# Kernel tuning notes

Measured on AMD Instinct MI355X. Metric: run time of the kernel, lower is better.

## Reference

```python
import jax, jax.numpy as jnp
import numpy as np

N = 100000; E = 1600000; D_IN = 9; HID = 16; HEADS = 8; D = HID * HEADS; G = 1000
NEG_SLOPE = 0.2; LN_EPS = 1e-5


def _gat_conv(x, src, dst, W, a_src, a_dst, b, heads, ch):
    # PyG GATConv (eval mode, self-loops already appended to src/dst)
    h = (x @ W).reshape(-1, heads, ch)                   # [N,H,C]
    al_s = (h * a_src).sum(-1)                           # [N,H]
    al_d = (h * a_dst).sum(-1)                           # [N,H]
    e = al_s[src] + al_d[dst]                            # [Et,H]
    e = jnp.where(e > 0, e, NEG_SLOPE * e)               # LeakyReLU(0.2)
    m = jax.ops.segment_max(e, dst, num_segments=N)      # per-dst softmax
    alpha = jnp.exp(e - m[dst])
    denom = jax.ops.segment_sum(alpha, dst, num_segments=N)
    alpha = alpha / (denom[dst] + 1e-16)
    out = jax.ops.segment_sum(h[src] * alpha[:, :, None], dst, num_segments=N)
    return out.reshape(-1, heads * ch) + b


def _ln_graph(x, g, b):
    # PyG LayerNorm, mode='graph', batch=None: normalize over all nodes+channels
    mu = x.mean()
    var = jnp.mean((x - mu) ** 2)
    return (x - mu) / jnp.sqrt(var + LN_EPS) * g + b


def setup_inputs() -> dict:
    key = jax.random.key(0)
    ks = jax.random.split(key, 20)
    s = 0.1
    p = lambda i, shape: jax.random.normal(ks[i], shape, jnp.float32) * s
    return {
        "x": jax.random.normal(ks[0], (N, D_IN), jnp.float32),
        "edge_index": jax.random.randint(ks[1], (2, E), 0, N),
        "batch": jnp.sort(jax.random.randint(ks[2], (N,), 0, G)),
        "W1": p(3, (D_IN, D)), "a_src1": p(4, (HEADS, HID)), "a_dst1": p(5, (HEADS, HID)), "b1": jnp.zeros((D,), jnp.float32),
        "W2": p(6, (D, D)), "a_src2": p(7, (1, D)), "a_dst2": p(8, (1, D)), "b2": jnp.zeros((D,), jnp.float32),
        "fc1_w": p(9, (D, D)), "fc1_b": jnp.zeros((D,), jnp.float32),
        "fc2_w": p(10, (D, D)), "fc2_b": jnp.zeros((D,), jnp.float32),
        "fc3_w": p(11, (D, D)), "fc3_b": jnp.zeros((D,), jnp.float32),
        "fc4_w": p(12, (D, D)), "fc4_b": jnp.zeros((D,), jnp.float32),
        "g1": jnp.ones((D,), jnp.float32), "beta1": jnp.zeros((D,), jnp.float32),
        "g2": jnp.ones((D,), jnp.float32), "beta2": jnp.zeros((D,), jnp.float32),
        "fcf_w": p(13, (D, 1)), "fcf_b": jnp.zeros((1,), jnp.float32),
    }


def reference(x, edge_index, batch, W1, a_src1, a_dst1, b1, W2, a_src2, a_dst2, b2,
              fc1_w, fc1_b, fc2_w, fc2_b, fc3_w, fc3_b, fc4_w, fc4_b,
              g1, beta1, g2, beta2, fcf_w, fcf_b):
    loops = jnp.arange(N)
    src = jnp.concatenate([edge_index[0], loops])
    dst = jnp.concatenate([edge_index[1], loops])
    h = jax.nn.relu(_gat_conv(x, src, dst, W1, a_src1, a_dst1, b1, HEADS, HID))
    hc = h
    h = jax.nn.relu(h @ fc1_w + fc1_b)
    h = jax.nn.relu(h @ fc2_w + fc2_b + hc)
    h = _ln_graph(h, g1, beta1)
    hc = h
    h = _gat_conv(h, src, dst, W2, a_src2, a_dst2, b2, 1, D)
    h = jax.nn.relu(h @ fc3_w + fc3_b)
    h = h @ fc4_w + fc4_b + hc
    h = _ln_graph(h, g2, beta2)
    h = h @ fcf_w + fcf_b                                # [N,1]
    sums = jax.ops.segment_sum(h, batch, num_segments=G)
    cnt = jax.ops.segment_sum(jnp.ones((N,), h.dtype), batch, num_segments=G)
    return sums / jnp.maximum(cnt, 1.0)[:, None]          # global_mean_pool -> [G,1]
```

## Files before the change

kernel.cpp:

```cpp
#include <hip/hip_runtime.h>
#include <cstdint>

#define NN 100000
#define NE 1600000
#define DI 9
#define DD 128
#define NH 8
#define NG 1000
#define LOG2E 1.44269504f

#define NBK 3125
#define NBLK 256
#define EPB (NE/NBLK)

typedef unsigned int uint;
typedef __attribute__((ext_vector_type(8))) short bf16x8;
typedef __attribute__((ext_vector_type(4))) float f32x4;

__device__ __forceinline__ float leaky(float x){ return fmaxf(x, 0.2f*x); }
__device__ __forceinline__ uint f2bf(float f){
  uint u = __float_as_uint(f);
  return (u + 0x7fffu + ((u>>16)&1u)) >> 16;
}
__device__ __forceinline__ float bflo(uint p){ return __uint_as_float(p << 16); }
__device__ __forceinline__ float bfhi(uint p){ return __uint_as_float(p & 0xffff0000u); }
__device__ __forceinline__ uint packbf(float a, float b){ return f2bf(a) | (f2bf(b)<<16); }
__device__ __forceinline__ float rdlanef(float v, int l){
  return __uint_as_float((uint)__builtin_amdgcn_readlane((int)__float_as_uint(v), l));
}

union U16 { uint4 u; bf16x8 v; };
__device__ __forceinline__ bf16x8 ld8(const uint* p){ U16 t; t.u = *(const uint4*)p; return t.v; }

__global__ __launch_bounds__(512) void k_hist(const int* __restrict__ dst, int* __restrict__ hist){
  __shared__ int h[NBK];
  for (int i = threadIdx.x; i < NBK; i += 512) h[i] = 0;
  __syncthreads();
  int blk = blockIdx.x;
  int beg = blk*EPB, end = beg + EPB;
  for (int i = beg + threadIdx.x; i < end; i += 512)
    atomicAdd(&h[dst[i] >> 5], 1);
  __syncthreads();
  for (int b = threadIdx.x; b < NBK; b += 512) hist[(size_t)blk*NBK + b] = h[b];
}

__global__ __launch_bounds__(256) void k_bsum(int* __restrict__ hist, int* __restrict__ bsum){
  int b = blockIdx.x*256 + threadIdx.x;
  if (b >= NBK) return;
  int run = 0;
  for (int k = 0; k < NBLK; ++k){
    int t = hist[(size_t)k*NBK + b];
    hist[(size_t)k*NBK + b] = run;
    run += t;
  }
  bsum[b] = run;
}

__global__ __launch_bounds__(1024) void k_bscan(const int* __restrict__ bsum, int* __restrict__ bbase){
  __shared__ int sh[1024];
  __shared__ int carry;
  if (threadIdx.x == 0) carry = 0;
  __syncthreads();
  for (int c0 = 0; c0 < NBK; c0 += 1024){
    int i = c0 + threadIdx.x;
    int v = (i < NBK) ? bsum[i] : 0;
    sh[threadIdx.x] = v;
    __syncthreads();
    for (int off = 1; off < 1024; off <<= 1){
      int t = (threadIdx.x >= off) ? sh[threadIdx.x-off] : 0;
      __syncthreads();
      sh[threadIdx.x] += t;
      __syncthreads();
    }
    if (i < NBK) bbase[i] = carry + sh[threadIdx.x] - v;
    __syncthreads();
    if (threadIdx.x == 0) carry += sh[1023];
    __syncthreads();
  }
}

__global__ __launch_bounds__(512) void k_part(const int* __restrict__ src, const int* __restrict__ dst,
    const int* __restrict__ hist, const int* __restrict__ bbase, uint* __restrict__ ebuf){
  __shared__ int cur[NBK];
  int blk = blockIdx.x;
  for (int b = threadIdx.x; b < NBK; b += 512)
    cur[b] = hist[(size_t)blk*NBK + b] + bbase[b];
  __syncthreads();
  int beg = blk*EPB, end = beg + EPB;
  for (int i = beg + threadIdx.x; i < end; i += 512){
    int d = dst[i], s = src[i];
    int b = d >> 5;
    int p = atomicAdd(&cur[b], 1);
    ebuf[p] = (uint)s | ((uint)(d & 31) << 26);
  }
}

__global__ __launch_bounds__(64) void k_fin(const uint* __restrict__ ebuf, const int* __restrict__ bbase,
    const int* __restrict__ bsum, int* __restrict__ rowptr, int* __restrict__ col){
  __shared__ int cnt32[32];
  __shared__ int exc[32];
  int b = blockIdx.x;
  int lane = threadIdx.x;
  if (lane < 32) cnt32[lane] = 0;
  __syncthreads();
  int base = bbase[b], n = bsum[b];
  for (int i = lane; i < n; i += 64)
    atomicAdd(&cnt32[ebuf[base+i] >> 26], 1);
  __syncthreads();
  if (lane == 0){
    int run = 0;
    for (int d = 0; d < 32; ++d){
      int t = cnt32[d];
      exc[d] = run;
      rowptr[b*32 + d] = base + run;
      run += t;
    }
  }
  __syncthreads();
  if (lane < 32) cnt32[lane] = exc[lane];
  __syncthreads();
  for (int i = lane; i < n; i += 64){
    uint e = ebuf[base+i];
    int d = e >> 26;
    int r = atomicAdd(&cnt32[d], 1);
    col[base + r] = (int)(e & 0x03ffffffu);
  }
  if (b == 0 && lane == 0) rowptr[NN] = NE;
}

__global__ __launch_bounds__(64) void k_wconv5(const float* __restrict__ w0, const float* __restrict__ w1,
    const float* __restrict__ w2, const float* __restrict__ w3, const float* __restrict__ w4,
    uint* __restrict__ o0, uint* __restrict__ o1, uint* __restrict__ o2,
    uint* __restrict__ o3, uint* __restrict__ o4){
  int which = blockIdx.x >> 7;
  int n = blockIdx.x & 127;
  int t = threadIdx.x;
  const float* W = (which==0)?w0:(which==1)?w1:(which==2)?w2:(which==3)?w3:w4;
  uint* WT = (which==0)?o0:(which==1)?o1:(which==2)?o2:(which==3)?o3:o4;
  float a = W[(2*t)*DD + n];
  float b = W[(2*t+1)*DD + n];
  WT[n*64 + t] = packbf(a, b);
}

__global__ __launch_bounds__(128) void k_lin1(const float* __restrict__ x, const float* __restrict__ W1,
    const float* __restrict__ as1, const float* __restrict__ ad1,
    uint* __restrict__ t1b, float* __restrict__ al_s, float* __restrict__ al_d){
  int n = blockIdx.x;
  int c = threadIdx.x;
  const float* xr = x + n*DI;
  float t = 0.f;
  #pragma unroll
  for (int k = 0; k < DI; ++k) t = fmaf(xr[k], W1[k*DD+c], t);
  uint mybf = f2bf(t);
  uint pbf  = (uint)__shfl_xor((int)mybf, 1, 64);
  if (!(c & 1)) t1b[(size_t)n*64 + (c>>1)] = mybf | (pbf<<16);
  float vs = t * as1[c];
  float vd = t * ad1[c];
  #pragma unroll
  for (int m = 8; m >= 1; m >>= 1){ vs += __shfl_xor(vs, m, 16); vd += __shfl_xor(vd, m, 16); }
  if ((c & 15) == 0){
    al_s[n*NH + (c>>4)] = vs*LOG2E;
    al_d[n*NH + (c>>4)] = vd*LOG2E;
  }
}

__global__ __launch_bounds__(256) void k_gat1(const uint* __restrict__ t1b,
    const float* __restrict__ al_s, const float* __restrict__ al_d,
    const int* __restrict__ rowptr, const int* __restrict__ col,
    const float* __restrict__ b1, uint* __restrict__ outb){
  int n = blockIdx.x*4 + (threadIdx.x >> 6);
  if (n >= NN) return;
  uint lane = threadIdx.x & 63;
  uint h = lane >> 3;
  float ald = al_d[(uint)n*NH + h];
  float a0  = exp2f(leaky(al_s[(uint)n*NH + h] + ald));
  uint  ps  = t1b[(uint)n*64u + lane];
  float den = a0;
  float s0 = a0*bflo(ps), s1 = a0*bfhi(ps);
  int beg = rowptr[n], end = rowptr[n+1];
  for (int e = beg; e < end; e += 16){
    uint cs[16]; float ls[16]; uint pp[16];
    #pragma unroll
    for (int j = 0; j < 16; ++j) cs[j] = (uint)col[e + j];
    #pragma unroll
    for (int j = 0; j < 16; ++j){
      ls[j] = al_s[cs[j]*8u + h];
      pp[j] = t1b[cs[j]*64u + lane];
    }
    #pragma unroll
    for (int j = 0; j < 16; ++j){
      float a = (e + j < end) ? exp2f(leaky(ls[j] + ald)) : 0.f;
      den += a;
      s0 = fmaf(a, bflo(pp[j]), s0);
      s1 = fmaf(a, bfhi(pp[j]), s1);
    }
  }
  float inv = 1.f/(den + 1e-16f);
  float2 bb = ((const float2*)b1)[lane];
  outb[(uint)n*64u + lane] = packbf(fmaxf(s0*inv + bb.x, 0.f), fmaxf(s1*inv + bb.y, 0.f));
}

__global__ __launch_bounds__(256) void k_gat2(const uint* __restrict__ t2b,
    const float* __restrict__ al_s, const float* __restrict__ al_d,
    const int* __restrict__ rowptr, const int* __restrict__ col,
    const float* __restrict__ b2, uint* __restrict__ outb){
  int n = blockIdx.x*4 + (threadIdx.x >> 6);
  if (n >= NN) return;
  uint lane = threadIdx.x & 63;
  float ald = al_d[n];
  float a0  = exp2f(leaky(al_s[n] + ald));
  uint  ps  = t2b[(uint)n*64u + lane];
  float s0 = a0*bflo(ps), s1 = a0*bfhi(ps);
  float vden = 0.f;
  int beg = rowptr[n], end = rowptr[n+1];
  for (int e = beg; e < end; e += 64){
    int ej = e + (int)lane;
    uint  mc = (uint)col[ej];
    float ml = al_s[mc];
    float ma = (ej < end) ? exp2f(leaky(ml + ald)) : 0.f;
    vden += ma;
    int rem = end - e;
    #pragma unroll
    for (int jb = 0; jb < 4; ++jb){
      if (jb*16 < rem){
        #pragma unroll
        for (int j = 0; j < 16; ++j){
          int lsrc = jb*16 + j;
          float a = rdlanef(ma, lsrc);
          uint  c = (uint)__builtin_amdgcn_readlane((int)mc, lsrc);
          uint  p = t2b[c*64u + lane];
          s0 = fmaf(a, bflo(p), s0);
          s1 = fmaf(a, bfhi(p), s1);
        }
      }
    }
  }
  #pragma unroll
  for (int m = 32; m >= 1; m >>= 1) vden += __shfl_xor(vden, m, 64);
  float inv = 1.f/(a0 + vden + 1e-16f);
  float2 bb = ((const float2*)b2)[lane];
  outb[(uint)n*64u + lane] = packbf(s0*inv + bb.x, s1*inv + bb.y);
}

template<bool RELU, bool BIAS, bool RES, bool LNRED, bool AL2>
__global__ __launch_bounds__(256) void k_mfma(const uint* __restrict__ Xb, const uint* __restrict__ WTb,
    const float* __restrict__ bias, const uint* __restrict__ resb, uint* __restrict__ outb,
    float* __restrict__ pbuf, const float* __restrict__ avs, const float* __restrict__ avd,
    float* __restrict__ o_als, float* __restrict__ o_ald, int nrows){
  int lane = threadIdx.x & 63;
  int wid  = threadIdx.x >> 6;
  int m0 = blockIdx.x*128 + wid*32;
  int lr = lane & 15, hi4 = lane >> 4;
  f32x4 acc[2][8];
  #pragma unroll
  for (int a = 0; a < 2; ++a)
    #pragma unroll
    for (int c = 0; c < 8; ++c) acc[a][c] = (f32x4){0.f,0.f,0.f,0.f};
  int ra0 = m0 + lr;      if (ra0 > NN-1) ra0 = NN-1;
  int ra1 = m0 + 16 + lr; if (ra1 > NN-1) ra1 = NN-1;
  #pragma unroll
  for (int kk = 0; kk < 4; ++kk){
    int ko = kk*16 + hi4*4;
    bf16x8 a0 = ld8(Xb + (size_t)ra0*64 + ko);
    bf16x8 a1 = ld8(Xb + (size_t)ra1*64 + ko);
    #pragma unroll
    for (int c = 0; c < 8; ++c){
      bf16x8 b = ld8(WTb + (size_t)(c*16 + lr)*64 + ko);
      acc[0][c] = __builtin_amdgcn_mfma_f32_16x16x32_bf16(a0, b, acc[0][c], 0, 0, 0);
      acc[1][c] = __builtin_amdgcn_mfma_f32_16x16x32_bf16(a1, b, acc[1][c], 0, 0, 0);
    }
  }
  if (AL2){
    #pragma unroll
    for (int rg = 0; rg < 2; ++rg){
      #pragma unroll
      for (int r = 0; r < 4; ++r){
        float vs = 0.f, vd = 0.f;
        #pragma unroll
        for (int c = 0; c < 8; ++c){
          float v = acc[rg][c][r];
          vs = fmaf(v, avs[c*16 + lr], vs);
          vd = fmaf(v, avd[c*16 + lr], vd);
        }
        #pragma unroll
        for (int m = 8; m >= 1; m >>= 1){ vs += __shfl_xor(vs, m, 64); vd += __shfl_xor(vd, m, 64); }
        int row = m0 + rg*16 + hi4*4 + r;
        if (lr == 0 && row < nrows){ o_als[row] = vs*LOG2E; o_ald[row] = vd*LOG2E; }
      }
    }
  }
  bool evn = !(lane & 1);
  int cph = lr >> 1;
  float lns = 0.f, lnss = 0.f;
  #pragma unroll
  for (int rg = 0; rg < 2; ++rg){
    #pragma unroll
    for (int c = 0; c < 8; ++c){
      int cp = c*8 + cph;
      #pragma unroll
      for (int r = 0; r < 4; ++r){
        float v0 = acc[rg][c][r];
        float v1 = __shfl_xor(v0, 1, 64);
        int row = m0 + rg*16 + hi4*4 + r;
        if (evn && row < nrows){
          if (BIAS){ float2 bb = ((const float2*)bias)[cp]; v0 += bb.x; v1 += bb.y; }
          if (RES){ uint rr = resb[(size_t)row*64 + cp]; v0 += bflo(rr); v1 += bfhi(rr); }
          if (RELU){ v0 = fmaxf(v0, 0.f); v1 = fmaxf(v1, 0.f); }
          outb[(size_t)row*64 + cp] = packbf(v0, v1);
          if (LNRED){ lns += v0 + v1; lnss += v0*v0 + v1*v1; }
        }
      }
    }
  }
  if (LNRED){
    #pragma unroll
    for (int m = 32; m >= 1; m >>= 1){ lns += __shfl_xor(lns, m, 64); lnss += __shfl_xor(lnss, m, 64); }
    __shared__ float shred[8];
    if (lane == 0){ shred[wid*2] = lns; shred[wid*2+1] = lnss; }
    __syncthreads();
    if (threadIdx.x == 0){
      float S = 0.f, SS = 0.f;
      for (int w = 0; w < 4; ++w){ S += shred[2*w]; SS += shred[2*w+1]; }
      pbuf[blockIdx.x*2] = S; pbuf[blockIdx.x*2+1] = SS;
    }
  }
}

__global__ __launch_bounds__(256) void k_ln_stats(const float* __restrict__ pbuf, float* __restrict__ stats, int nb){
  float s = 0.f, ss = 0.f;
  for (int i = threadIdx.x; i < nb; i += 256){ s += pbuf[2*i]; ss += pbuf[2*i+1]; }
  #pragma unroll
  for (int m = 32; m >= 1; m >>= 1){ s += __shfl_xor(s, m, 64); ss += __shfl_xor(ss, m, 64); }
  __shared__ float sh[8];
  int wid = threadIdx.x >> 6, lane = threadIdx.x & 63;
  if (lane == 0){ sh[wid*2] = s; sh[wid*2+1] = ss; }
  __syncthreads();
  if (threadIdx.x == 0){
    float S = 0.f, SS = 0.f;
    for (int w = 0; w < 4; ++w){ S += sh[2*w]; SS += sh[2*w+1]; }
    const float inv = 1.f/((float)NN*(float)DD);
    float mu = S*inv;
    float var = SS*inv - mu*mu;
    stats[0] = mu;
    stats[1] = rsqrtf(var + 1e-5f);
  }
}

__global__ __launch_bounds__(256) void k_ln_apply_bf(uint* __restrict__ xb, const float* __restrict__ g,
    const float* __restrict__ be, const float* __restrict__ stats){
  const int n4 = NN*16;
  float mu = stats[0], rs = stats[1];
  uint4* x4 = (uint4*)xb;
  const float2* g2 = (const float2*)g;
  const float2* b2 = (const float2*)be;
  for (int i = blockIdx.x*256 + threadIdx.x; i < n4; i += gridDim.x*256){
    int cb = (i & 15)*4;
    uint4 u = x4[i];
    float2 ga = g2[cb],   gb = g2[cb+1], gc = g2[cb+2], gd = g2[cb+3];
    float2 ba = b2[cb],   bb = b2[cb+1], bc = b2[cb+2], bd = b2[cb+3];
    u.x = packbf((bflo(u.x)-mu)*rs*ga.x + ba.x, (bfhi(u.x)-mu)*rs*ga.y + ba.y);
    u.y = packbf((bflo(u.y)-mu)*rs*gb.x + bb.x, (bfhi(u.y)-mu)*rs*gb.y + bb.y);
    u.z = packbf((bflo(u.z)-mu)*rs*gc.x + bc.x, (bfhi(u.z)-mu)*rs*gc.y + bc.y);
    u.w = packbf((bflo(u.w)-mu)*rs*gd.x + bd.x, (bfhi(u.w)-mu)*rs*gd.y + bd.y);
    x4[i] = u;
  }
}

__global__ __launch_bounds__(256) void k_fdot_ln(const uint* __restrict__ xb, const float* __restrict__ g,
    const float* __restrict__ be, const float* __restrict__ stats,
    const float* __restrict__ fw, const float* __restrict__ fb, float* __restrict__ val){
  int n = blockIdx.x*4 + (threadIdx.x >> 6);
  if (n >= NN) return;
  int lane = threadIdx.x & 63;
  float mu = stats[0], rs = stats[1];
  uint p = xb[(size_t)n*64 + lane];
  float2 gg = ((const float2*)g)[lane];
  float2 bb = ((const float2*)be)[lane];
  float2 ww = ((const float2*)fw)[lane];
  float v = ((bflo(p)-mu)*rs*gg.x + bb.x)*ww.x + ((bfhi(p)-mu)*rs*gg.y + bb.y)*ww.y;
  #pragma unroll
  for (int m = 32; m >= 1; m >>= 1) v += __shfl_xor(v, m, 64);
  if (lane == 0) val[n] = v + fb[0];
}

__global__ __launch_bounds__(64) void k_pool(const float* __restrict__ val, const int* __restrict__ batch,
                                             float* __restrict__ out){
  int g = blockIdx.x;
  int lane = threadIdx.x;
  int lo = 0, hi = NN;
  while (lo < hi){ int mid = (lo+hi)>>1; if (batch[mid] < g) lo = mid+1; else hi = mid; }
  int start = lo;
  hi = NN;
  while (lo < hi){ int mid = (lo+hi)>>1; if (batch[mid] < g+1) lo = mid+1; else hi = mid; }
  int end = lo;
  float s = 0.f;
  for (int i = start + lane; i < end; i += 64) s += val[i];
  #pragma unroll
  for (int m = 32; m >= 1; m >>= 1) s += __shfl_xor(s, m, 64);
  if (lane == 0) out[g] = s / fmaxf((float)(end - start), 1.f);
}

extern "C" void kernel_launch(void* const* d_in, const int* in_sizes, int n_in,
                              void* d_out, int out_size, void* d_ws, size_t ws_size,
                              hipStream_t stream){
  const float* x   = (const float*)d_in[0];
  const int*   ei  = (const int*)d_in[1];
  const int* batch = (const int*)d_in[2];
  const float* W1  = (const float*)d_in[3];
  const float* as1 = (const float*)d_in[4];
  const float* ad1 = (const float*)d_in[5];
  const float* b1  = (const float*)d_in[6];
  const float* W2  = (const float*)d_in[7];
  const float* as2 = (const float*)d_in[8];
  const float* ad2 = (const float*)d_in[9];
  const float* b2  = (const float*)d_in[10];
  const float* fc1w= (const float*)d_in[11];
  const float* fc1b= (const float*)d_in[12];
  const float* fc2w= (const float*)d_in[13];
  const float* fc2b= (const float*)d_in[14];
  const float* fc3w= (const float*)d_in[15];
  const float* fc3b= (const float*)d_in[16];
  const float* fc4w= (const float*)d_in[17];
  const float* fc4b= (const float*)d_in[18];
  const float* g1  = (const float*)d_in[19];
  const float* be1 = (const float*)d_in[20];
  const float* g2  = (const float*)d_in[21];
  const float* be2 = (const float*)d_in[22];
  const float* fcw = (const float*)d_in[23];
  const float* fcb = (const float*)d_in[24];
  float* out = (float*)d_out;
  (void)in_sizes; (void)n_in; (void)out_size; (void)ws_size;

  char* ws = (char*)d_ws;
  size_t off = 0;
  auto alloc = [&](size_t bytes)->void*{
    void* p = ws + off;
    off += (bytes + 255) & ~(size_t)255;
    return p;
  };
  float* A    = (float*)alloc((size_t)NN*DD*4);
  float* B    = (float*)alloc((size_t)NN*DD*4);
  float* C    = (float*)alloc((size_t)NN*DD*4);
  float* als1 = (float*)alloc((size_t)NN*NH*4);
  float* ald1 = (float*)alloc((size_t)NN*NH*4);
  float* als2 = (float*)alloc((size_t)NN*4);
  float* ald2 = (float*)alloc((size_t)NN*4);
  float* escr = (float*)alloc((size_t)NE*4);
  int*   rowptr = (int*)alloc((size_t)(NN+1)*4);
  int*   col    = (int*)alloc((size_t)(NE+64)*4);
  int*   bsum   = (int*)alloc((size_t)NBK*4);
  int*   bbase  = (int*)alloc((size_t)NBK*4);
  float* pbuf   = (float*)alloc(1024*2*4);
  float* stats  = (float*)alloc(2*4);
  float* val    = (float*)alloc((size_t)NN*4);
  uint* wt_fc1  = (uint*)alloc((size_t)DD*64*4);
  uint* wt_fc2  = (uint*)alloc((size_t)DD*64*4);
  uint* wt_w2   = (uint*)alloc((size_t)DD*64*4);
  uint* wt_fc3  = (uint*)alloc((size_t)DD*64*4);
  uint* wt_fc4  = (uint*)alloc((size_t)DD*64*4);

  uint*  Ab     = (uint*)A;
  uint*  Bb     = (uint*)B;
  uint*  Cb     = (uint*)C;
  int*   hist   = (int*)A;
  uint*  ebuf   = (uint*)escr;

  const int* esrc = ei;
  const int* edst = ei + NE;

  hipMemsetAsync(col + NE, 0, 64*4, stream);

  k_hist <<<NBLK, 512, 0, stream>>>(edst, hist);
  k_bsum <<<(NBK+255)/256, 256, 0, stream>>>(hist, bsum);
  k_bscan<<<1, 1024, 0, stream>>>(bsum, bbase);
  k_part <<<NBLK, 512, 0, stream>>>(esrc, edst, hist, bbase, ebuf);
  k_fin  <<<NBK, 64, 0, stream>>>(ebuf, bbase, bsum, rowptr, col);

  k_wconv5<<<5*DD, 64, 0, stream>>>(fc1w, fc2w, W2, fc3w, fc4w,
                                    wt_fc1, wt_fc2, wt_w2, wt_fc3, wt_fc4);

  const int WB = (NN + 3)/4;
  const int GB = (NN + 127)/128;

  k_lin1<<<NN, 128, 0, stream>>>(x, W1, as1, ad1, Ab, als1, ald1);
  k_gat1<<<WB, 256, 0, stream>>>(Ab, als1, ald1, rowptr, col, b1, Bb);

  k_mfma<true,  true, false, false, false><<<GB, 256, 0, stream>>>(Bb, wt_fc1, fc1b, nullptr, Ab, nullptr, nullptr, nullptr, nullptr, nullptr, NN);
  k_mfma<true,  true, true,  true,  false><<<GB, 256, 0, stream>>>(Ab, wt_fc2, fc2b, Bb,      Cb, pbuf,    nullptr, nullptr, nullptr, nullptr, NN);

  k_ln_stats<<<1, 256, 0, stream>>>(pbuf, stats, GB);
  k_ln_apply_bf<<<1024, 256, 0, stream>>>(Cb, g1, be1, stats);

  k_mfma<false, false, false, false, true ><<<GB, 256, 0, stream>>>(Cb, wt_w2, nullptr, nullptr, Ab, nullptr, as2, ad2, als2, ald2, NN);
  k_gat2<<<WB, 256, 0, stream>>>(Ab, als2, ald2, rowptr, col, b2, Bb);

  k_mfma<true,  true, false, false, false><<<GB, 256, 0, stream>>>(Bb, wt_fc3, fc3b, nullptr, Ab, nullptr, nullptr, nullptr, nullptr, nullptr, NN);
  k_mfma<false, true, true,  true,  false><<<GB, 256, 0, stream>>>(Ab, wt_fc4, fc4b, Cb,      Bb, pbuf,    nullptr, nullptr, nullptr, nullptr, NN);

  k_ln_stats<<<1, 256, 0, stream>>>(pbuf, stats, GB);
  k_fdot_ln<<<WB, 256, 0, stream>>>(Bb, g2, be2, stats, fcw, fcb, val);
  k_pool<<<NG, 64, 0, stream>>>(val, batch, out);
}
```

Before: 477.8 us.

## Coarsen CSR radix buckets to 512 nodes and scan bucket offsets in shared memory

The CSR build now partitions edges into 196 buckets of 512 destination nodes instead of 3125 buckets of 32. That shrinks the per-block histograms, the bucket-sum pass and the bucket-offset scan (now a single 1024-wide pass). k_fin now runs 256 threads per bucket and computes the 512 per-node offsets with a parallel shared-memory prefix scan. The packed edge format moves to 20 bits of source and 9 bits of local destination. The gat2 column load is also clamped so tail lanes no longer read past the row end. The trade-off is fewer, larger blocks in k_fin, which may lower parallelism for that pass, and more atomic contention on each shared counter.

```diff
diff --git a/kernel.cpp b/kernel.cpp
--- a/kernel.cpp
+++ b/kernel.cpp
@@ -9,7 +9,7 @@
 #define NG 1000
 #define LOG2E 1.44269504f
 
-#define NBK 3125
+#define NBK 196
 #define NBLK 256
 #define EPB (NE/NBLK)
 
@@ -39,9 +39,9 @@
   int blk = blockIdx.x;
   int beg = blk*EPB, end = beg + EPB;
   for (int i = beg + threadIdx.x; i < end; i += 512)
-    atomicAdd(&h[dst[i] >> 5], 1);
-  __syncthreads();
-  for (int b = threadIdx.x; b < NBK; b += 512) hist[(size_t)blk*NBK + b] = h[b];
+    atomicAdd(&h[dst[i] >> 9], 1);
+  __syncthreads();
+  for (int b = threadIdx.x; b < NBK; b += 512) hist[blk*NBK + b] = h[b];
 }
 
 __global__ __launch_bounds__(256) void k_bsum(int* __restrict__ hist, int* __restrict__ bsum){
@@ -49,8 +49,8 @@
   if (b >= NBK) return;
   int run = 0;
   for (int k = 0; k < NBLK; ++k){
-    int t = hist[(size_t)k*NBK + b];
-    hist[(size_t)k*NBK + b] = run;
+    int t = hist[k*NBK + b];
+    hist[k*NBK + b] = run;
     run += t;
   }
   bsum[b] = run;
@@ -58,25 +58,17 @@
 
 __global__ __launch_bounds__(1024) void k_bscan(const int* __restrict__ bsum, int* __restrict__ bbase){
   __shared__ int sh[1024];
-  __shared__ int carry;
-  if (threadIdx.x == 0) carry = 0;
-  __syncthreads();
-  for (int c0 = 0; c0 < NBK; c0 += 1024){
-    int i = c0 + threadIdx.x;
-    int v = (i < NBK) ? bsum[i] : 0;
-    sh[threadIdx.x] = v;
+  int i = threadIdx.x;
+  int v = (i < NBK) ? bsum[i] : 0;
+  sh[i] = v;
+  __syncthreads();
+  for (int off = 1; off < 1024; off <<= 1){
+    int t = (i >= off) ? sh[i-off] : 0;
     __syncthreads();
-    for (int off = 1; off < 1024; off <<= 1){
-      int t = (threadIdx.x >= off) ? sh[threadIdx.x-off] : 0;
-      __syncthreads();
-      sh[threadIdx.x] += t;
-      __syncthreads();
-    }
-    if (i < NBK) bbase[i] = carry + sh[threadIdx.x] - v;
+    sh[i] += t;
     __syncthreads();
-    if (threadIdx.x == 0) carry += sh[1023];
-    __syncthreads();
-  }
+  }
+  if (i < NBK) bbase[i] = sh[i] - v;
 }
 
 __global__ __launch_bounds__(512) void k_part(const int* __restrict__ src, const int* __restrict__ dst,
@@ -84,48 +76,55 @@
   __shared__ int cur[NBK];
   int blk = blockIdx.x;
   for (int b = threadIdx.x; b < NBK; b += 512)
-    cur[b] = hist[(size_t)blk*NBK + b] + bbase[b];
+    cur[b] = hist[blk*NBK + b] + bbase[b];
   __syncthreads();
   int beg = blk*EPB, end = beg + EPB;
   for (int i = beg + threadIdx.x; i < end; i += 512){
     int d = dst[i], s = src[i];
-    int b = d >> 5;
+    int b = d >> 9;
     int p = atomicAdd(&cur[b], 1);
-    ebuf[p] = (uint)s | ((uint)(d & 31) << 26);
-  }
-}
-
-__global__ __launch_bounds__(64) void k_fin(const uint* __restrict__ ebuf, const int* __restrict__ bbase,
+    ebuf[p] = (uint)s | ((uint)(d & 511) << 20);
+  }
+}
+
+__global__ __launch_bounds__(256) void k_fin(const uint* __restrict__ ebuf, const int* __restrict__ bbase,
     const int* __restrict__ bsum, int* __restrict__ rowptr, int* __restrict__ col){
-  __shared__ int cnt32[32];
-  __shared__ int exc[32];
+  __shared__ int cnt[512];
+  __shared__ int sc[256];
   int b = blockIdx.x;
-  int lane = threadIdx.x;
-  if (lane < 32) cnt32[lane] = 0;
+  int t = threadIdx.x;
+  int nb0 = b*512;
+  int nodes = NN - nb0; if (nodes > 512) nodes = 512;
+  cnt[t] = 0; cnt[t+256] = 0;
   __syncthreads();
   int base = bbase[b], n = bsum[b];
-  for (int i = lane; i < n; i += 64)
-    atomicAdd(&cnt32[ebuf[base+i] >> 26], 1);
-  __syncthreads();
-  if (lane == 0){
-    int run = 0;
-    for (int d = 0; d < 32; ++d){
-      int t = cnt32[d];
-      exc[d] = run;
-      rowptr[b*32 + d] = base + run;
-      run += t;
-    }
-  }
-  __syncthreads();
-  if (lane < 32) cnt32[lane] = exc[lane];
-  __syncthreads();
-  for (int i = lane; i < n; i += 64){
+  for (int i = t; i < n; i += 256)
+    atomicAdd(&cnt[ebuf[base+i] >> 20], 1);
+  __syncthreads();
+  int a0 = cnt[2*t], a1 = cnt[2*t+1];
+  int pairsum = a0 + a1;
+  sc[t] = pairsum;
+  __syncthreads();
+  for (int off = 1; off < 256; off <<= 1){
+    int v = (t >= off) ? sc[t-off] : 0;
+    __syncthreads();
+    sc[t] += v;
+    __syncthreads();
+  }
+  int excl = sc[t] - pairsum;
+  __syncthreads();
+  cnt[2*t]   = excl;
+  cnt[2*t+1] = excl + a0;
+  if (2*t   < nodes) rowptr[nb0 + 2*t]   = base + excl;
+  if (2*t+1 < nodes) rowptr[nb0 + 2*t+1] = base + excl + a0;
+  __syncthreads();
+  for (int i = t; i < n; i += 256){
     uint e = ebuf[base+i];
-    int d = e >> 26;
-    int r = atomicAdd(&cnt32[d], 1);
-    col[base + r] = (int)(e & 0x03ffffffu);
-  }
-  if (b == 0 && lane == 0) rowptr[NN] = NE;
+    int d = (int)(e >> 20);
+    int r = atomicAdd(&cnt[d], 1);
+    col[base + r] = (int)(e & 0xFFFFFu);
+  }
+  if (b == 0 && t == 0) rowptr[NN] = NE;
 }
 
 __global__ __launch_bounds__(64) void k_wconv5(const float* __restrict__ w0, const float* __restrict__ w1,
@@ -215,7 +214,7 @@
   int beg = rowptr[n], end = rowptr[n+1];
   for (int e = beg; e < end; e += 64){
     int ej = e + (int)lane;
-    uint  mc = (uint)col[ej];
+    uint  mc = (uint)col[(ej < end) ? ej : (end-1)];
     float ml = al_s[mc];
     float ma = (ej < end) ? exp2f(leaky(ml + ald)) : 0.f;
     vden += ma;
@@ -474,7 +473,7 @@
   k_bsum <<<(NBK+255)/256, 256, 0, stream>>>(hist, bsum);
   k_bscan<<<1, 1024, 0, stream>>>(bsum, bbase);
   k_part <<<NBLK, 512, 0, stream>>>(esrc, edst, hist, bbase, ebuf);
-  k_fin  <<<NBK, 64, 0, stream>>>(ebuf, bbase, bsum, rowptr, col);
+  k_fin  <<<NBK, 256, 0, stream>>>(ebuf, bbase, bsum, rowptr, col);
 
   k_wconv5<<<5*DD, 64, 0, stream>>>(fc1w, fc2w, W2, fc3w, fc4w,
                                     wt_fc1, wt_fc2, wt_w2, wt_fc3, wt_fc4);
```

After: 467.4 us. -2.2%, faster.
